# Performance work log

Measured on AMD Instinct MI355X. Metric: run time of the kernel, lower is better.

Reference implementation:

```python
import jax, jax.numpy as jnp
import numpy as np

E = 512   # embed_size
H = 8     # num_heads
D = E // H
N = 4
T = 2048


def quantize(x, b, e):
    # fake-quant: scale by 2^e, clamp to signed b-bit range, floor, dequant
    s = jnp.exp2(e)
    lo = -jnp.exp2(b - 1.0)
    hi = jnp.exp2(b - 1.0) - 1.0
    return jnp.floor(jnp.clip(x / s, lo, hi)) * s


def setup_inputs() -> dict:
    key = jax.random.key(0)
    ks = jax.random.split(key, 8)
    f = lambda k, shape: jax.random.normal(k, shape, dtype=jnp.float32)
    w = 1.0 / np.sqrt(E)  # ~ torch Linear init scale
    return {
        "values": f(ks[0], (N, T, E)),
        "keys": f(ks[1], (N, T, E)),
        "query": f(ks[2], (N, T, E)),
        "Wq": f(ks[3], (E, E)) * w, "bq": jnp.zeros((E,), jnp.float32),
        "Wk": f(ks[4], (E, E)) * w, "bk": jnp.zeros((E,), jnp.float32),
        "Wv": f(ks[5], (E, E)) * w, "bv": jnp.zeros((E,), jnp.float32),
        "Wo": f(ks[6], (E, E)) * w, "bo": jnp.zeros((E,), jnp.float32),
        "b_param": jnp.float32(8.0),
        "e_param": jnp.float32(0.0),
    }


def reference(values, keys, query, Wq, bq, Wk, bk, Wv, bv, Wo, bo, b_param, e_param):
    n, t, emb = query.shape
    d = emb // H
    # linear projections (torch Linear: x @ W^T + b), split heads -> [N,H,T,D]
    q = (query @ Wq.T + bq).reshape(n, t, H, d).transpose(0, 2, 1, 3)
    k = (keys @ Wk.T + bk).reshape(n, t, H, d).transpose(0, 2, 1, 3)
    v = (values @ Wv.T + bv).reshape(n, t, H, d).transpose(0, 2, 1, 3)
    b = jnp.clip(b_param, 1.0, 8.0)
    q = quantize(q, b, e_param)
    k = quantize(k, b, e_param)
    v = quantize(v, b, e_param)
    # NOTE: source scales by sqrt(embed_size), not sqrt(head_dim)
    energy = jnp.einsum('nhqd,nhkd->nhqk', q, k) / jnp.sqrt(jnp.float32(emb))
    attn = jax.nn.softmax(energy, axis=-1)
    out = jnp.einsum('nhqk,nhkd->nhqd', attn, v)
    out = out.transpose(0, 2, 1, 3).reshape(n, t, emb)
    return out @ Wo.T + bo
```

## Files before the change

### kernel.cpp

```cpp
#include <hip/hip_runtime.h>
#include <hip/hip_bf16.h>
#include <hip/hip_fp16.h>
#include <cstdint>
#include <cstddef>


typedef __attribute__((ext_vector_type(8))) _Float16 f16x8;
typedef __attribute__((ext_vector_type(2))) __fp16 hf16x2;
typedef __attribute__((ext_vector_type(16))) float f32x16;
typedef __attribute__((ext_vector_type(4))) unsigned u32x4;
typedef unsigned short u16;

#define EL  4194304
#define WEL 262144

static __device__ __forceinline__ u16 f2h(float x) {
  _Float16 h = (_Float16)x;
  return __builtin_bit_cast(u16, h);
}
static __device__ __forceinline__ unsigned pkh2(float a, float b) {
  hf16x2 p = __builtin_amdgcn_cvt_pkrtz(a, b);
  return __builtin_bit_cast(unsigned, p);
}
static __device__ __forceinline__ void gl_lds16(const void* g, void* l) {
  __builtin_amdgcn_global_load_lds(
      (__attribute__((address_space(1))) void*)g,
      (__attribute__((address_space(3))) void*)l, 16, 0, 0);
}

struct PrepAllArgs { const float* src[7]; };

__global__ __launch_bounds__(256) void prep_all_kernel(PrepAllArgs a,
                                                       u16* __restrict__ dst)
{
  const int i = blockIdx.x * 256 + threadIdx.x;
  const float* src; int off;
  if (i < 3145728) {
    const int m = i >> 20; off = i & 1048575;
    src = (m == 0) ? a.src[0] : (m == 1) ? a.src[1] : a.src[2];
  } else {
    const int j = i - 3145728; const int w = j >> 16; off = j & 65535;
    src = (w == 0) ? a.src[3] : (w == 1) ? a.src[4]
        : (w == 2) ? a.src[5] : a.src[6];
  }
  const float4 v = ((const float4*)src)[off];
  ushort4 o;
  o.x = f2h(v.x); o.y = f2h(v.y); o.z = f2h(v.z); o.w = f2h(v.w);
  ((ushort4*)dst)[i] = o;
}

struct ProjArgs {
  const u16* X[3]; const u16* W[3]; const float* bias[3];
  u16* dst[3]; int trans[3];
};

__global__ __launch_bounds__(256, 3) void proj_kernel(ProjArgs args,
    const float* __restrict__ bparam, const float* __restrict__ eparam)
{
  __shared__ u16 sm[17408];
  u16* const As = sm;
  u16* const Bs = sm + 8192;

  const int z = blockIdx.z;
  const u16* __restrict__ X = args.X[z];
  const u16* __restrict__ W = args.W[z];
  const float* __restrict__ bias = args.bias[z];
  u16* __restrict__ dst = args.dst[z];
  const int mode = args.trans[z];

  const int tid  = threadIdx.x;
  const int lane = tid & 63;
  const int wave = tid >> 6;
  const int lam  = lane & 31;
  const int hl   = lane >> 5;
  const int wm   = wave & 1;
  const int wn   = wave >> 1;
  const int mbase = blockIdx.x * 128;
  const int nbase = blockIdx.y * 128;

  const int srow = tid >> 3;
  const int sj   = (tid & 7) ^ (srow & 7);
  const u16* gA = X + (size_t)(mbase + srow) * 512 + sj * 8;
  const u16* gB = W + (size_t)(nbase + srow) * 512 + sj * 8;

  int offA[2][4], offB[2][4];
#pragma unroll
  for (int f = 0; f < 2; ++f)
#pragma unroll
    for (int kk = 0; kk < 4; ++kk) {
      const int c = 2 * kk + hl;
      const int m = wm * 64 + f * 32 + lam;
      offA[f][kk] = m * 128 + ((c ^ (m & 7)) * 16);
      const int nn = wn * 64 + f * 32 + lam;
      offB[f][kk] = nn * 128 + ((c ^ (nn & 7)) * 16);
    }

  f32x16 acc[2][2];
#pragma unroll
  for (int a = 0; a < 2; ++a)
#pragma unroll
    for (int b = 0; b < 2; ++b)
#pragma unroll
      for (int i = 0; i < 16; ++i) acc[a][b][i] = 0.f;

  for (int kt = 0; kt < 512; kt += 64) {
    __syncthreads();
#pragma unroll
    for (int t = 0; t < 4; ++t) {
      gl_lds16(gA + kt + t * 32 * 512, (char*)As + tid * 16 + t * 4096);
      gl_lds16(gB + kt + t * 32 * 512, (char*)Bs + tid * 16 + t * 4096);
    }
    __syncthreads();

    f16x8 fA[2][4], fB[2][4];
#pragma unroll
    for (int f = 0; f < 2; ++f)
#pragma unroll
      for (int kk = 0; kk < 4; ++kk) {
        fA[f][kk] = *(const f16x8*)((const char*)As + offA[f][kk]);
        fB[f][kk] = *(const f16x8*)((const char*)Bs + offB[f][kk]);
      }
#pragma unroll
    for (int mf = 0; mf < 2; ++mf)
#pragma unroll
      for (int nf = 0; nf < 2; ++nf)
#pragma unroll
        for (int kk = 0; kk < 4; ++kk)
          acc[mf][nf] = __builtin_amdgcn_mfma_f32_32x32x16_f16(
              fA[mf][kk], fB[nf][kk], acc[mf][nf], 0, 0, 0);
  }

  const float bq   = fminf(fmaxf(bparam[0], 1.0f), 8.0f);
  const float e    = eparam[0];
  const float s    = exp2f(e);
  const float invs = exp2f(-e);
  const float qlo  = -exp2f(bq - 1.0f);
  const float qhi  = exp2f(bq - 1.0f) - 1.0f;
  const int nidx = mbase >> 11;
  const int tb   = mbase & 2047;
  const int hb   = nbase >> 6;

  if (mode == 0) {
#pragma unroll
    for (int mf = 0; mf < 2; ++mf)
#pragma unroll
      for (int nf = 0; nf < 2; ++nf)
#pragma unroll
        for (int reg = 0; reg < 16; ++reg) {
          int col = wn * 64 + nf * 32 + lam;
          int row = wm * 64 + mf * 32 + (reg & 3) + 8 * (reg >> 2) + 4 * hl;
          float v = acc[mf][nf][reg] + bias[nbase + col];
          float qv = floorf(fminf(fmaxf(v * invs, qlo), qhi)) * s;
          dst[((size_t)(nidx * 8 + hb + (col >> 6)) * 2048 + tb + row) * 64 +
              (col & 63)] = f2h(qv);
        }
  } else if (mode == 1) {
#pragma unroll
    for (int mf = 0; mf < 2; ++mf)
#pragma unroll
      for (int nf = 0; nf < 2; ++nf)
#pragma unroll
        for (int reg = 0; reg < 16; ++reg) {
          int col = wn * 64 + nf * 32 + lam;
          int row = wm * 64 + mf * 32 + (reg & 3) + 8 * (reg >> 2) + 4 * hl;
          float v = acc[mf][nf][reg] + bias[nbase + col];
          float qv = floorf(fminf(fmaxf(v * invs, qlo), qhi)) * s;
          const int t = tb + row;
          const int d = col & 63;
          dst[(size_t)(nidx * 8 + hb + (col >> 6)) * 131072 +
              (t >> 5) * 2048 + (t & 31) * 64 + (((d >> 3) ^ (t & 7)) << 3) +
              (d & 7)] = f2h(qv);
        }
  } else {
    __syncthreads();
#pragma unroll
    for (int mf = 0; mf < 2; ++mf)
#pragma unroll
      for (int nf = 0; nf < 2; ++nf)
#pragma unroll
        for (int reg = 0; reg < 16; ++reg) {
          int col = wn * 64 + nf * 32 + lam;
          int row = wm * 64 + mf * 32 + (reg & 3) + 8 * (reg >> 2) + 4 * hl;
          float v = acc[mf][nf][reg] + bias[nbase + col];
          float qv = floorf(fminf(fmaxf(v * invs, qlo), qhi)) * s;
          sm[col * 136 + row] = f2h(qv);
        }
    __syncthreads();
    const int r = tid >> 1, half = tid & 1;
    const u16* sp = sm + r * 136 + half * 64;
    const int d = r & 63;
    const int dsw = d & 3;
    u16* const gp0 = dst + (size_t)(nidx * 8 + hb + (r >> 6)) * 131072;
#pragma unroll
    for (int i = 0; i < 8; ++i) {
      const int t = tb + half * 64 + i * 8;
      *(uint4*)(gp0 + (t >> 5) * 2048 + d * 32 +
                ((((t >> 3) & 3) ^ dsw) << 3)) = *(const uint4*)(sp + i * 8);
    }
  }
}

__global__ __launch_bounds__(256, 2) void attn_kernel(
    const u16* __restrict__ qbuf, const u16* __restrict__ kbuf,
    const u16* __restrict__ vtbuf, u16* __restrict__ ctx)
{
  __shared__ u16 sm[25088];
  char* const smc = (char*)sm;

  const int tid  = threadIdx.x;
  const int wave = tid >> 6;
  const int lane = tid & 63;
  const int lam  = lane & 31;
  const int hl   = lane >> 5;
  const int qt = blockIdx.x, hd = blockIdx.y, n = blockIdx.z;
  const int nh = n * 8 + hd;
  const int qbase = qt * 64;

  const u16* Qp = qbuf + ((size_t)nh * 2048 + qbase) * 64;
  const u16* gK = kbuf  + (size_t)nh * 131072 + wave * 2048 + lane * 8;
  const u16* gV = vtbuf + (size_t)nh * 131072 + wave * 2048 + lane * 8;
  char* const kvb = smc + wave * 12288;

  f16x8 qf[2][4];
#pragma unroll
  for (int qb = 0; qb < 2; ++qb)
#pragma unroll
    for (int dk = 0; dk < 4; ++dk)
      qf[qb][dk] = *(const f16x8*)(Qp + (qb * 32 + lam) * 64 + dk * 16 + hl * 8);
#pragma unroll
  for (int qb = 0; qb < 2; ++qb)
#pragma unroll
    for (int dk = 0; dk < 4; ++dk)
      asm volatile("" :: "v"(qf[qb][dk]));

  auto stage4 = [&](const u16* src, char* dstb) {
#pragma unroll
    for (int r = 0; r < 4; ++r)
      gl_lds16(src + r * 512, dstb + r * 1024 + lane * 16);
  };

  stage4(gK,        kvb);
  stage4(gV,        kvb + 8192);
  stage4(gK + 8192, kvb + 4096);

  int offK[4];
#pragma unroll
  for (int dk = 0; dk < 4; ++dk)
    offK[dk] = lam * 128 + (((2 * dk + hl) ^ (lam & 7)) << 4);
  int offV[2][2];
#pragma unroll
  for (int nf = 0; nf < 2; ++nf)
#pragma unroll
    for (int kkl = 0; kkl < 2; ++kkl) {
      const int d = nf * 32 + lam;
      offV[nf][kkl] = 8192 + d * 64 + (((2 * kkl + hl) ^ (d & 3)) << 4);
    }

  const float sc = (float)(1.4426950408889634 / 22.627416997969522);

  float l_acc[2] = {0.f, 0.f};
  f32x16 O[2][2];
#pragma unroll
  for (int a = 0; a < 2; ++a)
#pragma unroll
    for (int b = 0; b < 2; ++b)
#pragma unroll
      for (int i = 0; i < 16; ++i) O[a][b][i] = 0.f;

  for (int t = 0; t < 16; ++t) {
    char* const kb = kvb + (t & 1) * 4096;
    asm volatile("s_waitcnt vmcnt(8)" ::: "memory");
    f16x8 Kf[4];
#pragma unroll
    for (int dk = 0; dk < 4; ++dk)
      Kf[dk] = *(const f16x8*)(kb + offK[dk]);

    f16x8 pfrag[2][2];
#pragma unroll
    for (int qb = 0; qb < 2; ++qb) {
      f32x16 S;
#pragma unroll
      for (int i = 0; i < 16; ++i) S[i] = 0.f;
#pragma unroll
      for (int dk = 0; dk < 4; ++dk)
        S = __builtin_amdgcn_mfma_f32_32x32x16_f16(Kf[dk], qf[qb][dk],
                                                   S, 0, 0, 0);
      unsigned pk[4][2];
#pragma unroll
      for (int gh = 0; gh < 4; ++gh) {
        float p0 = __builtin_amdgcn_exp2f(S[4 * gh + 0] * sc);
        float p1 = __builtin_amdgcn_exp2f(S[4 * gh + 1] * sc);
        float p2 = __builtin_amdgcn_exp2f(S[4 * gh + 2] * sc);
        float p3 = __builtin_amdgcn_exp2f(S[4 * gh + 3] * sc);
        l_acc[qb] += (p0 + p1) + (p2 + p3);
        pk[gh][0] = pkh2(p0, p1);
        pk[gh][1] = pkh2(p2, p3);
      }
#pragma unroll
      for (int kkl = 0; kkl < 2; ++kkl) {
        unsigned s0 = hl ? pk[2 * kkl][0] : pk[2 * kkl + 1][0];
        unsigned s1 = hl ? pk[2 * kkl][1] : pk[2 * kkl + 1][1];
        unsigned o0 = hl ? pk[2 * kkl + 1][0] : pk[2 * kkl][0];
        unsigned o1 = hl ? pk[2 * kkl + 1][1] : pk[2 * kkl][1];
        unsigned rr0 = (unsigned)__shfl_xor((int)s0, 32);
        unsigned rr1 = (unsigned)__shfl_xor((int)s1, 32);
        u32x4 f;
        f[0] = hl ? rr0 : o0;
        f[1] = hl ? rr1 : o1;
        f[2] = hl ? o0 : rr0;
        f[3] = hl ? o1 : rr1;
        pfrag[qb][kkl] = __builtin_bit_cast(f16x8, f);
      }
    }

    asm volatile("s_waitcnt vmcnt(4)" ::: "memory");
    f16x8 Vf[2][2];
#pragma unroll
    for (int nf = 0; nf < 2; ++nf)
#pragma unroll
      for (int kkl = 0; kkl < 2; ++kkl)
        Vf[nf][kkl] = *(const f16x8*)(kvb + offV[nf][kkl]);
#pragma unroll
    for (int qb = 0; qb < 2; ++qb)
#pragma unroll
      for (int nf = 0; nf < 2; ++nf)
#pragma unroll
        for (int kkl = 0; kkl < 2; ++kkl)
          O[qb][nf] = __builtin_amdgcn_mfma_f32_32x32x16_f16(
              pfrag[qb][kkl], Vf[nf][kkl], O[qb][nf], 0, 0, 0);

    asm volatile("s_waitcnt lgkmcnt(0)" ::: "memory");
    stage4(gV + ((t + 1) & 15) * 8192, kvb + 8192);
    stage4(gK + ((t + 2) & 15) * 8192, kvb + (t & 1) * 4096);
  }

  asm volatile("s_waitcnt vmcnt(0)" ::: "memory");
#pragma unroll
  for (int qb = 0; qb < 2; ++qb) l_acc[qb] += __shfl_xor(l_acc[qb], 32);
  float* lred = (float*)(smc + 49152);
  if (hl == 0) {
    lred[wave * 64 + lam]      = l_acc[0];
    lred[wave * 64 + 32 + lam] = l_acc[1];
  }
  __syncthreads();

  const int q  = tid >> 3;
  const int dc = (tid & 7) * 8;
#pragma unroll
  for (int qb = 0; qb < 2; ++qb) {
    float* Ow = (float*)(smc + wave * 8704);
#pragma unroll
    for (int nf = 0; nf < 2; ++nf)
#pragma unroll
      for (int r = 0; r < 16; ++r) {
        const int qrow = (r & 3) + 8 * (r >> 2) + 4 * hl;
        Ow[qrow * 68 + nf * 32 + lam] = O[qb][nf][r];
      }
    __syncthreads();
    float a[8];
    {
      const char* b = smc + q * 272 + dc * 4;
      const float4 v0 = *(const float4*)b;
      const float4 v1 = *(const float4*)(b + 16);
      a[0] = v0.x; a[1] = v0.y; a[2] = v0.z; a[3] = v0.w;
      a[4] = v1.x; a[5] = v1.y; a[6] = v1.z; a[7] = v1.w;
    }
#pragma unroll
    for (int w = 1; w < 4; ++w) {
      const char* b = smc + w * 8704 + q * 272 + dc * 4;
      const float4 v0 = *(const float4*)b;
      const float4 v1 = *(const float4*)(b + 16);
      a[0] += v0.x; a[1] += v0.y; a[2] += v0.z; a[3] += v0.w;
      a[4] += v1.x; a[5] += v1.y; a[6] += v1.z; a[7] += v1.w;
    }
    const float lsum = lred[qb * 32 + q] + lred[64 + qb * 32 + q] +
                       lred[128 + qb * 32 + q] + lred[192 + qb * 32 + q];
    const float rinv = 1.0f / lsum;
    unsigned outp[4];
#pragma unroll
    for (int i = 0; i < 4; ++i)
      outp[i] = pkh2(a[2 * i] * rinv, a[2 * i + 1] * rinv);
    u16* cp = ctx + ((size_t)n * 2048 + qbase + qb * 32 + q) * 512 +
              hd * 64 + dc;
    *(uint4*)cp = *(const uint4*)outp;
    if (qb == 0) __syncthreads();
  }
}

__global__ __launch_bounds__(256) void outproj_kernel(
    const u16* __restrict__ ctxb, const u16* __restrict__ Wof,
    const float* __restrict__ bias, float* __restrict__ out)
{
  __shared__ u16 sm[12288];
  u16* const As = sm;
  u16* const Bs = sm + 4096;

  const int tid  = threadIdx.x;
  const int lane = tid & 63;
  const int wave = tid >> 6;
  const int lam  = lane & 31;
  const int hl   = lane >> 5;
  const int wm   = wave & 1;
  const int wn   = wave >> 1;
  const int mbase = blockIdx.x * 64;
  const int nbase = blockIdx.y * 128;

  const int srow = tid >> 3;
  const int sj   = (tid & 7) ^ (srow & 7);
  const u16* gA = ctxb + (size_t)(mbase + srow) * 512 + sj * 8;
  const u16* gB = Wof  + (size_t)(nbase + srow) * 512 + sj * 8;

  int offA[4], offB[2][4];
#pragma unroll
  for (int kk = 0; kk < 4; ++kk) {
    const int c = 2 * kk + hl;
    const int m = wm * 32 + lam;
    offA[kk] = m * 128 + ((c ^ (m & 7)) * 16);
#pragma unroll
    for (int f = 0; f < 2; ++f) {
      const int nn = wn * 64 + f * 32 + lam;
      offB[f][kk] = nn * 128 + ((c ^ (nn & 7)) * 16);
    }
  }

  f32x16 acc[2];
#pragma unroll
  for (int a = 0; a < 2; ++a)
#pragma unroll
    for (int i = 0; i < 16; ++i) acc[a][i] = 0.f;

  for (int kt = 0; kt < 512; kt += 64) {
    __syncthreads();
#pragma unroll
    for (int t = 0; t < 2; ++t)
      gl_lds16(gA + kt + t * 32 * 512, (char*)As + tid * 16 + t * 4096);
#pragma unroll
    for (int t = 0; t < 4; ++t)
      gl_lds16(gB + kt + t * 32 * 512, (char*)Bs + tid * 16 + t * 4096);
    __syncthreads();

    f16x8 fA[4], fB[2][4];
#pragma unroll
    for (int kk = 0; kk < 4; ++kk) {
      fA[kk] = *(const f16x8*)((const char*)As + offA[kk]);
#pragma unroll
      for (int f = 0; f < 2; ++f)
        fB[f][kk] = *(const f16x8*)((const char*)Bs + offB[f][kk]);
    }
#pragma unroll
    for (int nf = 0; nf < 2; ++nf)
#pragma unroll
      for (int kk = 0; kk < 4; ++kk)
        acc[nf] = __builtin_amdgcn_mfma_f32_32x32x16_f16(
            fA[kk], fB[nf][kk], acc[nf], 0, 0, 0);
  }

#pragma unroll
  for (int nf = 0; nf < 2; ++nf)
#pragma unroll
    for (int reg = 0; reg < 16; ++reg) {
      int col = nbase + wn * 64 + nf * 32 + lam;
      int row = mbase + wm * 32 + (reg & 3) + 8 * (reg >> 2) + 4 * hl;
      out[(size_t)row * 512 + col] = acc[nf][reg] + bias[col];
    }
}

extern "C" void kernel_launch(void* const* d_in, const int* in_sizes, int n_in,
                              void* d_out, int out_size, void* d_ws, size_t ws_size,
                              hipStream_t stream) {
  (void)in_sizes; (void)n_in; (void)out_size; (void)ws_size;
  const float* values = (const float*)d_in[0];
  const float* keys   = (const float*)d_in[1];
  const float* query  = (const float*)d_in[2];
  const float* Wq = (const float*)d_in[3];  const float* bq = (const float*)d_in[4];
  const float* Wk = (const float*)d_in[5];  const float* bk = (const float*)d_in[6];
  const float* Wv = (const float*)d_in[7];  const float* bv = (const float*)d_in[8];
  const float* Wo = (const float*)d_in[9];  const float* bo = (const float*)d_in[10];
  const float* bp = (const float*)d_in[11]; const float* ep = (const float*)d_in[12];

  u16* ws    = (u16*)d_ws;
  u16* qbuf  = ws;
  u16* kbuf  = ws + (size_t)EL;
  u16* vtbuf = ws + (size_t)2 * EL;
  u16* ctx   = ws + (size_t)3 * EL;
  u16* xwf   = ws + (size_t)4 * EL;

  PrepAllArgs pa;
  pa.src[0] = query; pa.src[1] = keys; pa.src[2] = values;
  pa.src[3] = Wq; pa.src[4] = Wk; pa.src[5] = Wv; pa.src[6] = Wo;
  prep_all_kernel<<<13312, 256, 0, stream>>>(pa, xwf);

  const float* Bsrc[3] = {bq, bk, bv};
  u16* Dst[3] = {qbuf, kbuf, vtbuf};
  ProjArgs a;
  for (int m = 0; m < 3; ++m) {
    a.X[m] = xwf + (size_t)m * EL;
    a.W[m] = xwf + (size_t)3 * EL + (size_t)m * WEL;
    a.bias[m] = Bsrc[m]; a.dst[m] = Dst[m]; a.trans[m] = m;
  }
  proj_kernel<<<dim3(64, 4, 3), 256, 0, stream>>>(a, bp, ep);

  attn_kernel<<<dim3(32, 8, 4), 256, 0, stream>>>(qbuf, kbuf, vtbuf, ctx);
  outproj_kernel<<<dim3(128, 4), 256, 0, stream>>>(
      ctx, xwf + (size_t)3 * EL + (size_t)3 * WEL, bo, (float*)d_out);
}
```

Before: 193.3 us.

## Shrink attention LDS staging to raise occupancy, remap blocks, add MFMA priority

The attention kernel drops from triple-buffered K/V staging to single K and V buffers per wave, cutting shared memory so four blocks can share a CU instead of two. The V^T layout written by the projection kernel changes to a new swizzle, and the attention V reads are updated to match. The grid becomes 1D with a remap that spreads consecutive blocks across heads, and s_setprio is raised around the MFMA sections. The cost is less prefetch depth: the next tile load now has to hide behind the current tile's compute, and the higher occupancy may put pressure on registers.

```diff
diff --git a/kernel.cpp b/kernel.cpp
--- a/kernel.cpp
+++ b/kernel.cpp
@@ -188,23 +188,26 @@
     __syncthreads();
     const int r = tid >> 1, half = tid & 1;
     const u16* sp = sm + r * 136 + half * 64;
-    const int d = r & 63;
-    const int dsw = d & 3;
-    u16* const gp0 = dst + (size_t)(nidx * 8 + hb + (r >> 6)) * 131072;
+    const int d  = r & 63;
+    const int sb = d & 1;
+    const int rx = (d >> 1) & 7;
+    u16* const gp0 = dst + (size_t)(nidx * 8 + hb + (r >> 6)) * 131072 +
+                     (d >> 1) * 64;
 #pragma unroll
     for (int i = 0; i < 8; ++i) {
       const int t = tb + half * 64 + i * 8;
-      *(uint4*)(gp0 + (t >> 5) * 2048 + d * 32 +
-                ((((t >> 3) & 3) ^ dsw) << 3)) = *(const uint4*)(sp + i * 8);
-    }
-  }
-}
-
-__global__ __launch_bounds__(256, 2) void attn_kernel(
+      const int c = (t & 31) >> 3;
+      const int s2 = ((c << 1) | sb) ^ rx;
+      *(uint4*)(gp0 + (t >> 5) * 2048 + s2 * 8) = *(const uint4*)(sp + i * 8);
+    }
+  }
+}
+
+__global__ __launch_bounds__(256, 4) void attn_kernel(
     const u16* __restrict__ qbuf, const u16* __restrict__ kbuf,
     const u16* __restrict__ vtbuf, u16* __restrict__ ctx)
 {
-  __shared__ u16 sm[25088];
+  __shared__ u16 sm[17920];
   char* const smc = (char*)sm;
 
   const int tid  = threadIdx.x;
@@ -212,14 +215,18 @@
   const int lane = tid & 63;
   const int lam  = lane & 31;
   const int hl   = lane >> 5;
-  const int qt = blockIdx.x, hd = blockIdx.y, n = blockIdx.z;
-  const int nh = n * 8 + hd;
+  const int bid = blockIdx.x;
+  const int wg  = (bid & 7) * 128 + (bid >> 3);
+  const int qt = wg & 31;
+  const int nh = wg >> 5;
+  const int hd = nh & 7;
+  const int n  = nh >> 3;
   const int qbase = qt * 64;
 
   const u16* Qp = qbuf + ((size_t)nh * 2048 + qbase) * 64;
   const u16* gK = kbuf  + (size_t)nh * 131072 + wave * 2048 + lane * 8;
   const u16* gV = vtbuf + (size_t)nh * 131072 + wave * 2048 + lane * 8;
-  char* const kvb = smc + wave * 12288;
+  char* const kvb = smc + wave * 8192;
 
   f16x8 qf[2][4];
 #pragma unroll
@@ -239,9 +246,8 @@
       gl_lds16(src + r * 512, dstb + r * 1024 + lane * 16);
   };
 
-  stage4(gK,        kvb);
-  stage4(gV,        kvb + 8192);
-  stage4(gK + 8192, kvb + 4096);
+  stage4(gK, kvb);
+  stage4(gV, kvb + 4096);
 
   int offK[4];
 #pragma unroll
@@ -252,8 +258,9 @@
   for (int nf = 0; nf < 2; ++nf)
 #pragma unroll
     for (int kkl = 0; kkl < 2; ++kkl) {
-      const int d = nf * 32 + lam;
-      offV[nf][kkl] = 8192 + d * 64 + (((2 * kkl + hl) ^ (d & 3)) << 4);
+      const int R = nf * 16 + (lam >> 1);
+      const int s2 = (((2 * kkl + hl) << 1) | (lam & 1)) ^ (R & 7);
+      offV[nf][kkl] = 4096 + R * 128 + s2 * 16;
     }
 
   const float sc = (float)(1.4426950408889634 / 22.627416997969522);
@@ -268,12 +275,13 @@
       for (int i = 0; i < 16; ++i) O[a][b][i] = 0.f;
 
   for (int t = 0; t < 16; ++t) {
-    char* const kb = kvb + (t & 1) * 4096;
-    asm volatile("s_waitcnt vmcnt(8)" ::: "memory");
+    asm volatile("s_waitcnt vmcnt(4)" ::: "memory");
     f16x8 Kf[4];
 #pragma unroll
     for (int dk = 0; dk < 4; ++dk)
-      Kf[dk] = *(const f16x8*)(kb + offK[dk]);
+      Kf[dk] = *(const f16x8*)(kvb + offK[dk]);
+    asm volatile("s_waitcnt lgkmcnt(0)" ::: "memory");
+    stage4(gK + ((t + 1) & 15) * 8192, kvb);
 
     f16x8 pfrag[2][2];
 #pragma unroll
@@ -281,10 +289,12 @@
       f32x16 S;
 #pragma unroll
       for (int i = 0; i < 16; ++i) S[i] = 0.f;
+      __builtin_amdgcn_s_setprio(1);
 #pragma unroll
       for (int dk = 0; dk < 4; ++dk)
         S = __builtin_amdgcn_mfma_f32_32x32x16_f16(Kf[dk], qf[qb][dk],
                                                    S, 0, 0, 0);
+      __builtin_amdgcn_s_setprio(0);
       unsigned pk[4][2];
 #pragma unroll
       for (int gh = 0; gh < 4; ++gh) {
@@ -320,6 +330,10 @@
 #pragma unroll
       for (int kkl = 0; kkl < 2; ++kkl)
         Vf[nf][kkl] = *(const f16x8*)(kvb + offV[nf][kkl]);
+    asm volatile("s_waitcnt lgkmcnt(0)" ::: "memory");
+    stage4(gV + ((t + 1) & 15) * 8192, kvb + 4096);
+
+    __builtin_amdgcn_s_setprio(1);
 #pragma unroll
     for (int qb = 0; qb < 2; ++qb)
 #pragma unroll
@@ -328,16 +342,13 @@
         for (int kkl = 0; kkl < 2; ++kkl)
           O[qb][nf] = __builtin_amdgcn_mfma_f32_32x32x16_f16(
               pfrag[qb][kkl], Vf[nf][kkl], O[qb][nf], 0, 0, 0);
-
-    asm volatile("s_waitcnt lgkmcnt(0)" ::: "memory");
-    stage4(gV + ((t + 1) & 15) * 8192, kvb + 8192);
-    stage4(gK + ((t + 2) & 15) * 8192, kvb + (t & 1) * 4096);
+    __builtin_amdgcn_s_setprio(0);
   }
 
   asm volatile("s_waitcnt vmcnt(0)" ::: "memory");
 #pragma unroll
   for (int qb = 0; qb < 2; ++qb) l_acc[qb] += __shfl_xor(l_acc[qb], 32);
-  float* lred = (float*)(smc + 49152);
+  float* lred = (float*)(smc + 34816);
   if (hl == 0) {
     lred[wave * 64 + lam]      = l_acc[0];
     lred[wave * 64 + 32 + lam] = l_acc[1];
@@ -500,7 +511,7 @@
   }
   proj_kernel<<<dim3(64, 4, 3), 256, 0, stream>>>(a, bp, ep);
 
-  attn_kernel<<<dim3(32, 8, 4), 256, 0, stream>>>(qbuf, kbuf, vtbuf, ctx);
+  attn_kernel<<<dim3(1024), 256, 0, stream>>>(qbuf, kbuf, vtbuf, ctx);
   outproj_kernel<<<dim3(128, 4), 256, 0, stream>>>(
       ctx, xwf + (size_t)3 * EL + (size_t)3 * WEL, bo, (float*)d_out);
 }
```

Result: slower. 409.2 us (+111.7%).
